# Performance work log

Measured on AMD Instinct MI355X. Metric: run time of the kernel, lower is better.

## Reference

```python
import jax, jax.numpy as jnp
import numpy as np

N_TAGS = 128
ROOT = 126
END = 127
NEG = -10000.0


def setup_inputs() -> dict:
    key = jax.random.key(0)
    k1, k2, k3, k4 = jax.random.split(key, 4)
    bsz, T = 256, 256
    feats = jax.random.normal(k1, (bsz, T, N_TAGS), jnp.float32)
    tags = jax.random.randint(k2, (bsz, T), 0, ROOT)  # never ROOT/END
    lengths = jax.random.randint(k3, (bsz,), 1, T + 1)
    mask = (jnp.arange(T)[None, :] < lengths[:, None]).astype(jnp.int32)
    # xavier_normal_: std = gain * sqrt(2 / (fan_in + fan_out))
    std = np.float32(np.sqrt(2.0 / (2 * N_TAGS)))
    lt = jax.random.normal(k4, (N_TAGS, N_TAGS), jnp.float32) * std
    lt = lt.at[:, ROOT].set(NEG).at[END, :].set(NEG)
    return {"feats": feats, "tags": tags, "mask": mask, "log_transitions": lt}


def _neg_log_likelihood(feats, log_transitions, tags, maskf):
    bsz, T, n = feats.shape
    # ---- forward belief propagation (log partition) ----
    init = log_transitions[ROOT, :] + feats[:, 0, :]  # [b, n]

    def step(fv, xs):
        feat, m = xs  # feat: [b, n], m: [b]
        # logsumexp over previous tag axis; emission is independent of it
        nxt = jax.nn.logsumexp(fv[:, :, None] + log_transitions[None, :, :], axis=1) + feat
        return jnp.where(m[:, None] > 0, nxt, fv), None

    feats_t = jnp.swapaxes(feats, 0, 1)  # [T, b, n]
    fv, _ = jax.lax.scan(step, init, (feats_t[1:], maskf[:, 1:].T))
    partition = jax.nn.logsumexp(fv + log_transitions[:, END][None, :], axis=1)  # [b]

    # ---- gold path score ----
    trans_tt = log_transitions[tags[:, :-1], tags[:, 1:]]                         # [b, T-1]
    emis = jnp.take_along_axis(feats[:, :-1, :], tags[:, :-1, None], axis=2)[..., 0]
    scores = log_transitions[ROOT, tags[:, 0]]
    scores = scores + jnp.sum(trans_tt * maskf[:, 1:] + emis * maskf[:, :-1], axis=1)
    last_idx = (maskf.sum(axis=1) - 1.0).astype(jnp.int32)                         # [b]
    last_tags = jnp.take_along_axis(tags, last_idx[:, None], axis=1)[:, 0]
    last_input = jnp.take_along_axis(feats[:, -1, :], last_tags[:, None], axis=1)[:, 0]
    scores = scores + log_transitions[last_tags, END] + last_input * maskf[:, -1]

    return jnp.mean(partition - scores)


def reference(feats, tags, mask, log_transitions):
    maskf = mask.astype(feats.dtype)
    return _neg_log_likelihood(feats, log_transitions, tags, maskf)
```

## Files before the change

### kernel.cpp

```cpp
#include <hip/hip_runtime.h>
#include <hip/hip_bf16.h>

#define N_TAGS 128
#define T_LEN  256
#define BSZ    256
#define ROOT_T 126
#define END_T  127

typedef _Float16 h2 __attribute__((ext_vector_type(2)));
typedef int   i32x4 __attribute__((ext_vector_type(4)));

static __device__ __forceinline__ h2 pkrtz(float a, float b) {
  return __builtin_bit_cast(h2, __builtin_amdgcn_cvt_pkrtz(a, b));
}
static __device__ __forceinline__ float rfl(float x) {
  return __int_as_float(__builtin_amdgcn_readfirstlane(__float_as_int(x)));
}
static __device__ __forceinline__ h2 rdl(h2 v, int k) {
  return __builtin_bit_cast(h2, __builtin_amdgcn_readlane(__builtin_bit_cast(int, v), k));
}
static __device__ __forceinline__ float fdot2(h2 a, h2 b, float c) {
#if __has_builtin(__builtin_amdgcn_fdot2)
  return __builtin_amdgcn_fdot2(a, b, c, false);
#else
  float d;
  asm("v_dot2_f32_f16 %0, %1, %2, %3" : "=v"(d) : "v"(a), "v"(b), "v"(c));
  return d;
#endif
}
static __device__ __forceinline__ float wave_max(float x) {
  #pragma unroll
  for (int d = 1; d < 64; d <<= 1) x = fmaxf(x, __shfl_xor(x, d));
  return x;
}

static __device__ __forceinline__ void dotRL(h2 vp,
                                             const h2 (&EA)[64], const h2 (&EB)[64],
                                             float& s0, float& s1) {
  float a0=0.f,a1=0.f,a2=0.f,a3=0.f, b0=0.f,b1=0.f,b2=0.f,b3=0.f;
  #pragma unroll
  for (int q = 0; q < 64; q += 4) {
    const h2 u0 = rdl(vp, q + 0);
    const h2 u1 = rdl(vp, q + 1);
    const h2 u2 = rdl(vp, q + 2);
    const h2 u3 = rdl(vp, q + 3);
    a0 = fdot2(u0, EA[q + 0], a0);  b0 = fdot2(u0, EB[q + 0], b0);
    a1 = fdot2(u1, EA[q + 1], a1);  b1 = fdot2(u1, EB[q + 1], b1);
    a2 = fdot2(u2, EA[q + 2], a2);  b2 = fdot2(u2, EB[q + 2], b2);
    a3 = fdot2(u3, EA[q + 3], a3);  b3 = fdot2(u3, EB[q + 3], b3);
  }
  s0 = (a0 + a1) + (a2 + a3);
  s1 = (b0 + b1) + (b2 + b3);
}

__global__ void
__attribute__((amdgpu_flat_work_group_size(128, 128), amdgpu_waves_per_eu(1, 1)))
crf_fwd_kernel(
    const float* __restrict__ feats,
    const int*   __restrict__ tags,
    const int*   __restrict__ mask,
    const float* __restrict__ lt,
    float*       __restrict__ per_batch)
{
  const int b    = blockIdx.x;
  const int tid  = threadIdx.x;
  const int lane = tid & 63;
  const int wave = tid >> 6;

  __shared__ float stage[32 * 129];
  __shared__ float bb[N_TAGS];
  __shared__ float sred[2];

  const float* fb = feats + (size_t)b * T_LEN * N_TAGS;
  const int*   tb = tags  + b * T_LEN;

  int len;
  {
    const i32x4 mv = ((const i32x4*)(mask + b * T_LEN))[lane];
    int v = mv.x + mv.y + mv.z + mv.w;
    #pragma unroll
    for (int d = 1; d < 64; d <<= 1) v += __shfl_xor(v, d);
    len = __builtin_amdgcn_readfirstlane(v);
  }

  h2 EA[64], EB[64];
  #pragma unroll
  for (int c = 0; c < 4; ++c) {
    __syncthreads();
    #pragma unroll
    for (int rr = 0; rr < 32; ++rr)
      stage[rr * 129 + tid] = __expf(lt[(c * 32 + rr) * N_TAGS + tid]);
    __syncthreads();
    if (wave == 0) {
      #pragma unroll
      for (int k = 0; k < 16; ++k) {
        h2 ea, eb;
        ea.x = (_Float16)stage[(2*k)   * 129 + 2*lane];
        ea.y = (_Float16)stage[(2*k+1) * 129 + 2*lane];
        eb.x = (_Float16)stage[(2*k)   * 129 + 2*lane + 1];
        eb.y = (_Float16)stage[(2*k+1) * 129 + 2*lane + 1];
        EA[c*16 + k] = ea;
        EB[c*16 + k] = eb;
      }
    } else if ((lane >> 4) == c) {
      const int r0 = 2 * lane - 32 * c;
      #pragma unroll
      for (int q = 0; q < 64; ++q) {
        h2 ea, eb;
        ea.x = (_Float16)stage[r0       * 129 + 2*q];
        ea.y = (_Float16)stage[r0       * 129 + 2*q + 1];
        eb.x = (_Float16)stage[(r0 + 1) * 129 + 2*q];
        eb.y = (_Float16)stage[(r0 + 1) * 129 + 2*q + 1];
        EA[q] = ea;
        EB[q] = eb;
      }
    }
  }

  float st0, st1;

  if (wave == 0) {
    {
      const float2 f0 = ((const float2*)fb)[lane];
      st0 = lt[ROOT_T * N_TAGS + 2*lane]     + f0.x;
      st1 = lt[ROOT_T * N_TAGS + 2*lane + 1] + f0.y;
    }
    float2 fa = ((const float2*)(fb + 1 * N_TAGS))[lane];
    float2 fc = ((const float2*)(fb + 2 * N_TAGS))[lane];
    float2 fd = ((const float2*)(fb + 3 * N_TAGS))[lane];
    float m_cur = rfl(st0) + 2.0f;
    h2 vp = pkrtz(__expf(st0 - m_cur), __expf(st1 - m_cur));

    #pragma unroll 1
    for (int t = 1; t <= 128; ++t) {
      float s0, s1;
      dotRL(vp, EA, EB, s0, s1);
      const float nf0 = m_cur + __logf(s0) + fa.x;
      const float nf1 = m_cur + __logf(s1) + fa.y;
      const bool act = (t < len);
      st0 = act ? nf0 : st0;  st1 = act ? nf1 : st1;
      fa = fc;  fc = fd;
      fd = ((const float2*)(fb + (t + 3) * N_TAGS))[lane];
      const float m = rfl(st0) + 2.0f;
      vp = pkrtz(__expf(st0 - m), __expf(st1 - m));
      m_cur = m;
    }
  } else {
    st0 = lt[(2*lane)     * N_TAGS + END_T];
    st1 = lt[(2*lane + 1) * N_TAGS + END_T];
    float2 fw = ((const float2*)(fb + 255 * N_TAGS))[lane];
    float2 fa = ((const float2*)(fb + 254 * N_TAGS))[lane];
    float2 fc = ((const float2*)(fb + 253 * N_TAGS))[lane];
    float2 fd = ((const float2*)(fb + 252 * N_TAGS))[lane];
    const float y0i = st0 + fw.x, y1i = st1 + fw.y;
    float m_cur = rfl(y0i) + 2.0f;
    h2 vp = pkrtz(__expf(y0i - m_cur), __expf(y1i - m_cur));

    const int kmin = 256 - len;
    #pragma unroll 1
    for (int k = 0; k <= 127; ++k) {
      float s0, s1;
      dotRL(vp, EA, EB, s0, s1);
      const float nb0 = m_cur + __logf(s0);
      const float nb1 = m_cur + __logf(s1);
      const bool act = (k >= kmin) && (k <= 126);
      st0 = act ? nb0 : st0;  st1 = act ? nb1 : st1;
      const float w0 = fa.x, w1 = fa.y;
      fa = fc;  fc = fd;
      fd = ((const float2*)(fb + (251 - k) * N_TAGS))[lane];
      const float y0 = st0 + w0, y1 = st1 + w1;
      const float m = rfl(y0) + 2.0f;
      vp = pkrtz(__expf(y0 - m), __expf(y1 - m));
      m_cur = m;
    }
    bb[2*lane]     = st0;
    bb[2*lane + 1] = st1;
  }
  __syncthreads();

  float c = 0.f;
  #pragma unroll
  for (int q = 0; q < 2; ++q) {
    const int t  = tid + q * N_TAGS;
    const int tg = tb[t];
    if (t == 0)                           c += lt[ROOT_T * N_TAGS + tg];
    if (t >= 1 && t < len)                c += lt[tb[t - 1] * N_TAGS + tg];
    if (t < len && t <= T_LEN - 2)        c += fb[t * N_TAGS + tg];
    if (t == len - 1)                     c += lt[tg * N_TAGS + END_T];
    if (t == T_LEN - 1 && len == T_LEN)   c += fb[t * N_TAGS + tg];
  }
  #pragma unroll
  for (int d = 1; d < 64; d <<= 1) c += __shfl_xor(c, d);
  if (lane == 0) sred[wave] = c;

  float part = 0.f;
  if (wave == 0) {
    const float x0 = st0 + bb[2*lane];
    const float x1 = st1 + bb[2*lane + 1];
    const float mw = wave_max(fmaxf(x0, x1));
    float e = __expf(x0 - mw) + __expf(x1 - mw);
    #pragma unroll
    for (int d = 1; d < 64; d <<= 1) e += __shfl_xor(e, d);
    part = mw + __logf(e);
  }
  __syncthreads();

  if (tid == 0) per_batch[b] = part - (sred[0] + sred[1]);
}

__global__ __launch_bounds__(256) void crf_reduce_kernel(
    const float* __restrict__ per_batch, float* __restrict__ out)
{
  const int tid = threadIdx.x;
  float v = per_batch[tid] * (1.0f / BSZ);
  #pragma unroll
  for (int d = 1; d < 64; d <<= 1) v += __shfl_xor(v, d);
  __shared__ float r[4];
  if ((tid & 63) == 0) r[tid >> 6] = v;
  __syncthreads();
  if (tid == 0) out[0] = r[0] + r[1] + r[2] + r[3];
}

extern "C" void kernel_launch(void* const* d_in, const int* in_sizes, int n_in,
                              void* d_out, int out_size, void* d_ws, size_t ws_size,
                              hipStream_t stream) {
  (void)in_sizes; (void)n_in; (void)out_size; (void)ws_size;
  const float* feats = (const float*)d_in[0];
  const int*   tags  = (const int*)d_in[1];
  const int*   mask  = (const int*)d_in[2];
  const float* lt    = (const float*)d_in[3];
  float* per_batch = (float*)d_ws;

  crf_fwd_kernel<<<BSZ, 128, 0, stream>>>(feats, tags, mask, lt, per_batch);
  crf_reduce_kernel<<<1, 256, 0, stream>>>(per_batch, (float*)d_out);
}
```

Before: 78.73 us.

## Stage emission rows as fp16 in LDS before the forward/backward recurrences

Before the serial loops, all 128 threads cooperatively load emission rows 1..254, convert them to packed fp16 and store them in a 64KB LDS buffer. The recurrence loops then read emissions from LDS with a two-deep rotating prefetch instead of issuing global loads per step, and are unrolled by two. This is meant to take global-memory latency off the latency-bound per-timestep critical path. In exchange there is an up-front bulk load phase, fp16 rounding of emissions (precision loss), and much larger shared memory use.

```diff
diff --git a/kernel.cpp b/kernel.cpp
--- a/kernel.cpp
+++ b/kernel.cpp
@@ -8,6 +8,8 @@
 #define END_T  127
 
 typedef _Float16 h2 __attribute__((ext_vector_type(2)));
+typedef _Float16 h4 __attribute__((ext_vector_type(4)));
+typedef float f32x4 __attribute__((ext_vector_type(4)));
 typedef int   i32x4 __attribute__((ext_vector_type(4)));
 
 static __device__ __forceinline__ h2 pkrtz(float a, float b) {
@@ -67,9 +69,11 @@
   const int lane = tid & 63;
   const int wave = tid >> 6;
 
-  __shared__ float stage[32 * 129];
-  __shared__ float bb[N_TAGS];
-  __shared__ float sred[2];
+  __shared__ __align__(16) char smem[65536];
+  float* stage = (float*)smem;
+  #define FROW(r) ((h2*)smem + (size_t)((r) - 1) * 64)
+  float* bb   = (float*)(smem + 64000);
+  float* sred = (float*)(smem + 64520);
 
   const float* fb = feats + (size_t)b * T_LEN * N_TAGS;
   const int*   tb = tags  + b * T_LEN;
@@ -116,6 +120,22 @@
       }
     }
   }
+  __syncthreads();
+
+  {
+    const int j = tid & 31;
+    #pragma unroll 8
+    for (int it = 0; it < 64; ++it) {
+      const int r = it * 4 + (tid >> 5);
+      if (r >= 1 && r <= 254) {
+        const f32x4 v = ((const f32x4*)(fb + (size_t)r * N_TAGS))[j];
+        const h2 lo = pkrtz(v.x, v.y);
+        const h2 hi = pkrtz(v.z, v.w);
+        ((h4*)FROW(r))[j] = __builtin_shufflevector(lo, hi, 0, 1, 2, 3);
+      }
+    }
+  }
+  __syncthreads();
 
   float st0, st1;
 
@@ -125,22 +145,23 @@
       st0 = lt[ROOT_T * N_TAGS + 2*lane]     + f0.x;
       st1 = lt[ROOT_T * N_TAGS + 2*lane + 1] + f0.y;
     }
-    float2 fa = ((const float2*)(fb + 1 * N_TAGS))[lane];
-    float2 fc = ((const float2*)(fb + 2 * N_TAGS))[lane];
-    float2 fd = ((const float2*)(fb + 3 * N_TAGS))[lane];
+    h2 gb[2];
+    gb[1] = FROW(1)[lane];
+    gb[0] = FROW(2)[lane];
     float m_cur = rfl(st0) + 2.0f;
     h2 vp = pkrtz(__expf(st0 - m_cur), __expf(st1 - m_cur));
 
-    #pragma unroll 1
+    #pragma unroll 2
     for (int t = 1; t <= 128; ++t) {
       float s0, s1;
       dotRL(vp, EA, EB, s0, s1);
-      const float nf0 = m_cur + __logf(s0) + fa.x;
-      const float nf1 = m_cur + __logf(s1) + fa.y;
+      const h2 fa = gb[t & 1];
+      const int pr = (t + 2 <= 128) ? (t + 2) : 128;
+      gb[t & 1] = FROW(pr)[lane];
+      const float nf0 = m_cur + __logf(s0) + (float)fa.x;
+      const float nf1 = m_cur + __logf(s1) + (float)fa.y;
       const bool act = (t < len);
       st0 = act ? nf0 : st0;  st1 = act ? nf1 : st1;
-      fa = fc;  fc = fd;
-      fd = ((const float2*)(fb + (t + 3) * N_TAGS))[lane];
       const float m = rfl(st0) + 2.0f;
       vp = pkrtz(__expf(st0 - m), __expf(st1 - m));
       m_cur = m;
@@ -148,16 +169,16 @@
   } else {
     st0 = lt[(2*lane)     * N_TAGS + END_T];
     st1 = lt[(2*lane + 1) * N_TAGS + END_T];
-    float2 fw = ((const float2*)(fb + 255 * N_TAGS))[lane];
-    float2 fa = ((const float2*)(fb + 254 * N_TAGS))[lane];
-    float2 fc = ((const float2*)(fb + 253 * N_TAGS))[lane];
-    float2 fd = ((const float2*)(fb + 252 * N_TAGS))[lane];
+    const float2 fw = ((const float2*)(fb + 255 * N_TAGS))[lane];
+    h2 gb[2];
+    gb[0] = FROW(254)[lane];
+    gb[1] = FROW(253)[lane];
     const float y0i = st0 + fw.x, y1i = st1 + fw.y;
     float m_cur = rfl(y0i) + 2.0f;
     h2 vp = pkrtz(__expf(y0i - m_cur), __expf(y1i - m_cur));
 
     const int kmin = 256 - len;
-    #pragma unroll 1
+    #pragma unroll 2
     for (int k = 0; k <= 127; ++k) {
       float s0, s1;
       dotRL(vp, EA, EB, s0, s1);
@@ -165,10 +186,10 @@
       const float nb1 = m_cur + __logf(s1);
       const bool act = (k >= kmin) && (k <= 126);
       st0 = act ? nb0 : st0;  st1 = act ? nb1 : st1;
-      const float w0 = fa.x, w1 = fa.y;
-      fa = fc;  fc = fd;
-      fd = ((const float2*)(fb + (251 - k) * N_TAGS))[lane];
-      const float y0 = st0 + w0, y1 = st1 + w1;
+      const h2 fa = gb[k & 1];
+      const int pr = (252 - k >= 127) ? (252 - k) : 127;
+      gb[k & 1] = FROW(pr)[lane];
+      const float y0 = st0 + (float)fa.x, y1 = st1 + (float)fa.y;
       const float m = rfl(y0) + 2.0f;
       vp = pkrtz(__expf(y0 - m), __expf(y1 - m));
       m_cur = m;
```

New measurement: 92.27 us. +17.2%, slower.
